# Kernel optimization log

Hardware: AMD Instinct MI355X
Metric: run time of the kernel (lower is better)

## Reference

```python
import jax, jax.numpy as jnp
import numpy as np

# dims per init_kwargs / input_specs
B, C, H, W = 8, 256, 56, 56
K = 3            # kernel_size
S = 1            # stride
D = 1            # dilation
HEAD = 1
MID = int(C * 0.2)   # se_ratio bottleneck = 51
GAIN = float(np.sqrt(2.0))  # calculate_gain('relu')


def setup_inputs() -> dict:
    key = jax.random.key(0)
    ks = jax.random.split(key, 6)
    sc = 0.05
    return {
        "x": jax.random.normal(ks[0], (B, C, H, W), jnp.float32),
        # channel branch: 1x1 convs stored as dense matrices
        "w1": jax.random.normal(ks[1], (MID, C), jnp.float32) * sc,
        "b1": jnp.zeros((MID,), jnp.float32),
        "w2": jax.random.normal(ks[2], (C * K * K, MID), jnp.float32) * sc,
        "b2": jnp.zeros((C * K * K,), jnp.float32),
        # spatial branch: 1x1 conv c -> head*k^2
        "ws": jax.random.normal(ks[3], (HEAD * K * K, C), jnp.float32) * sc,
        "bs": jnp.zeros((HEAD * K * K,), jnp.float32),
        # FilterNorm running_std parameter (channel branch): randn * gain/k
        "fn_std": jax.random.normal(ks[4], (C * K * K,), jnp.float32) * (GAIN / K),
    }


def _ddf_mul(x, cf, sf):
    """Decoupled dynamic filter, 'mul' combine.
    x: (B,C,H,W), cf: (B,C,K,K) channel filter, sf: (B,K*K,Ho,Wo) spatial filter.
    out[b,c,i,j] = sum_{u,v} x[b,c, i*S+(u-(K-1)/2)*D, j*S+(v-(K-1)/2)*D] * cf[b,c,u,v] * sf[b,u*K+v,i,j]
    Accumulate over the K*K taps to avoid materializing the unfolded tensor."""
    p = D * (K - 1) // 2
    xp = jnp.pad(x, ((0, 0), (0, 0), (p, p), (p, p)))
    Ho, Wo = H // S, W // S
    out = jnp.zeros((B, C, Ho, Wo), x.dtype)
    for u in range(K):
        for v in range(K):
            patch = xp[:, :, u * D:u * D + S * Ho:S, v * D:v * D + S * Wo:S]
            out = out + patch * cf[:, :, u, v][:, :, None, None] * sf[:, u * K + v][:, None]
    return out


def reference(x, w1, b1, w2, b2, ws, bs, fn_std):
    # ---- channel branch: SE-style filter generation ----
    pooled = x.mean((2, 3))                                  # (B,C) global avg pool
    y = jax.nn.relu(pooled @ w1.T + b1)                      # (B,MID)
    y = (y @ w2.T + b2).reshape(B, C, K * K)                 # (B,C,K^2)
    # FilterNorm 'channel': normalize over K^2 (torch std -> ddof=1), learned std
    y = (y - y.mean(-1, keepdims=True)) / (y.std(-1, ddof=1, keepdims=True) + 1e-10)
    cf = (y.reshape(B, C * K * K) * fn_std).reshape(B, C, K, K)
    # ---- spatial branch: 1x1 conv (stride S) + FilterNorm 'spatial' ----
    xs = x[:, :, ::S, ::S]
    sf = jnp.einsum('bchw,nc->bnhw', xs, ws) + bs[None, :, None, None]  # (B,K^2,Ho,Wo)
    sf = sf.reshape(B, HEAD, K * K, H // S, W // S)
    sf = (sf - sf.mean(2, keepdims=True)) / (sf.std(2, ddof=1, keepdims=True) + 1e-10)
    sf = sf.reshape(B, HEAD * K * K, H // S, W // S) * (GAIN / K)
    # ---- fused per-pixel gather-multiply-reduce (head=1 -> no group reshape) ----
    return _ddf_mul(x, cf, sf)
```

## Files before the change

kernel.cpp:

```cpp
#include <hip/hip_runtime.h>
#include <math.h>

#define BB   8
#define CC   256
#define HH   56
#define WW   56
#define KK   3
#define MIDN 51
#define NTAP (KK*KK)
#define CKK  (CC*NTAP)
#define HW   (HH*WW)
#define NCH  8
#define CPC  (CC/NCH)
#define PBLK 13

__global__ __launch_bounds__(256) void pool_kernel(const float* __restrict__ x,
                                                   float* __restrict__ pooled) {
    int bc = blockIdx.x;
    const float* xp = x + (size_t)bc * HW;
    int t = threadIdx.x;
    float s = 0.f;
    for (int idx = t; idx < HW; idx += 256) s += xp[idx];
    for (int off = 32; off > 0; off >>= 1) s += __shfl_down(s, off, 64);
    __shared__ float red[4];
    int wave = t >> 6, lane = t & 63;
    if (lane == 0) red[wave] = s;
    __syncthreads();
    if (t == 0) pooled[bc] = (red[0] + red[1] + red[2] + red[3]) * (1.0f / HW);
}

__global__ __launch_bounds__(320) void mlp_kernel(const float* __restrict__ pooled,
                                                  const float* __restrict__ w1,
                                                  const float* __restrict__ b1,
                                                  const float* __restrict__ w2,
                                                  const float* __restrict__ b2,
                                                  const float* __restrict__ fn_std,
                                                  float* __restrict__ cf) {
    int blk = blockIdx.x;
    int b = blk >> 3, chunk = blk & 7;
    int c0 = chunk * 32;
    int t = threadIdx.x;
    __shared__ float ps[CC];
    __shared__ float y1[MIDN];
    __shared__ float y2s[32 * NTAP];
    if (t < CC) ps[t] = pooled[b * CC + t];
    __syncthreads();
    if (t < MIDN) {
        float acc = b1[t];
        const float* wr = w1 + t * CC;
        for (int c2 = 0; c2 < CC; ++c2) acc += ps[c2] * wr[c2];
        y1[t] = fmaxf(acc, 0.f);
    }
    __syncthreads();
    if (t < 32 * NTAP) {
        int cl = t / NTAP, q = t - cl * NTAP;
        int row = (c0 + cl) * NTAP + q;
        float acc = b2[row];
        const float* r = w2 + (size_t)row * MIDN;
        for (int m = 0; m < MIDN; ++m) acc += y1[m] * r[m];
        y2s[t] = acc;
    }
    __syncthreads();
    if (t < 32) {
        int c = c0 + t;
        float y2[NTAP];
        #pragma unroll
        for (int q = 0; q < NTAP; ++q) y2[q] = y2s[t * NTAP + q];
        float mean = 0.f;
        #pragma unroll
        for (int q = 0; q < NTAP; ++q) mean += y2[q];
        mean *= (1.f / NTAP);
        float var = 0.f;
        #pragma unroll
        for (int q = 0; q < NTAP; ++q) { float d = y2[q] - mean; var += d * d; }
        float inv = 1.f / (sqrtf(var * (1.f / (NTAP - 1))) + 1e-10f);
        #pragma unroll
        for (int q = 0; q < NTAP; ++q) {
            int idx = c * NTAP + q;
            cf[(size_t)b * CKK + idx] = (y2[q] - mean) * inv * fn_std[idx];
        }
    }
}

__global__ __launch_bounds__(256) void sfA_kernel(const float* __restrict__ x,
                                                  const float* __restrict__ ws,
                                                  float* __restrict__ partial) {
    int blk = blockIdx.x;
    int pb = blk % PBLK;
    int tmp = blk / PBLK;
    int chunk = tmp % NCH;
    int b = tmp / NCH;
    int t = threadIdx.x;
    __shared__ float wss[NTAP][CPC];
    for (int idx = t; idx < NTAP * CPC; idx += 256) {
        int n = idx / CPC, c = idx - n * CPC;
        wss[n][c] = ws[n * CC + chunk * CPC + c];
    }
    __syncthreads();
    int p = pb * 256 + t;
    if (p >= HW) return;
    float acc[NTAP];
    #pragma unroll
    for (int n = 0; n < NTAP; ++n) acc[n] = 0.f;
    const float* xp = x + ((size_t)(b * CC + chunk * CPC)) * HW + p;
    for (int c = 0; c < CPC; ++c) {
        float xv = xp[(size_t)c * HW];
        #pragma unroll
        for (int n = 0; n < NTAP; ++n) acc[n] += xv * wss[n][c];
    }
    float* pp = partial + ((size_t)((b * NCH + chunk) * NTAP)) * HW + p;
    #pragma unroll
    for (int n = 0; n < NTAP; ++n) pp[(size_t)n * HW] = acc[n];
}

__global__ __launch_bounds__(256) void sfB_kernel(const float* __restrict__ partial,
                                                  const float* __restrict__ bs,
                                                  float* __restrict__ sf) {
    int blk = blockIdx.x;
    int b = blk / PBLK, pb = blk % PBLK;
    int p = pb * 256 + threadIdx.x;
    if (p >= HW) return;
    float acc[NTAP];
    #pragma unroll
    for (int n = 0; n < NTAP; ++n) acc[n] = bs[n];
    const float* pp = partial + ((size_t)(b * NCH)) * NTAP * HW + p;
    for (int chunk = 0; chunk < NCH; ++chunk)
        #pragma unroll
        for (int n = 0; n < NTAP; ++n)
            acc[n] += pp[((size_t)(chunk * NTAP + n)) * HW];
    float mean = 0.f;
    #pragma unroll
    for (int n = 0; n < NTAP; ++n) mean += acc[n];
    mean *= (1.f / NTAP);
    float var = 0.f;
    #pragma unroll
    for (int n = 0; n < NTAP; ++n) { float d = acc[n] - mean; var += d * d; }
    float inv = 0.47140452079103173f /
                (sqrtf(var * (1.f / (NTAP - 1))) + 1e-10f);
    #pragma unroll
    for (int n = 0; n < NTAP; ++n)
        sf[((size_t)(b * NTAP + n)) * HW + p] = (acc[n] - mean) * inv;
}

__global__ __launch_bounds__(256) void ddf_kernel(const float* __restrict__ x,
                                                  const float* __restrict__ cf,
                                                  const float* __restrict__ sf,
                                                  float* __restrict__ out) {
    int bc = blockIdx.x;
    int b = bc / CC, c = bc % CC;
    int t = threadIdx.x;
    __shared__ float xt[58 * 58];
    for (int idx = t; idx < 58 * 58; idx += 256) xt[idx] = 0.f;
    __syncthreads();
    const float* xp = x + (size_t)bc * HW;
    for (int idx = t; idx < HW; idx += 256) {
        int r = idx / WW, col = idx - r * WW;
        xt[(r + 1) * 58 + col + 1] = xp[idx];
    }
    float cf9[NTAP];
    const float* cfp = cf + (size_t)b * CKK + c * NTAP;
    #pragma unroll
    for (int n = 0; n < NTAP; ++n) cf9[n] = cfp[n];
    __syncthreads();
    const float* sfb = sf + (size_t)b * NTAP * HW;
    float* op = out + (size_t)bc * HW;
    for (int idx = t; idx < HW; idx += 256) {
        int i = idx / WW, j = idx - (idx / WW) * WW;
        float acc = 0.f;
        #pragma unroll
        for (int u = 0; u < KK; ++u)
            #pragma unroll
            for (int v = 0; v < KK; ++v) {
                int n = u * KK + v;
                acc += xt[(i + u) * 58 + (j + v)] * cf9[n] * sfb[(size_t)n * HW + idx];
            }
        op[idx] = acc;
    }
}

extern "C" void kernel_launch(void* const* d_in, const int* in_sizes, int n_in,
                              void* d_out, int out_size, void* d_ws, size_t ws_size,
                              hipStream_t stream) {
    const float* x      = (const float*)d_in[0];
    const float* w1     = (const float*)d_in[1];
    const float* b1     = (const float*)d_in[2];
    const float* w2     = (const float*)d_in[3];
    const float* b2     = (const float*)d_in[4];
    const float* ws     = (const float*)d_in[5];
    const float* bs     = (const float*)d_in[6];
    const float* fn_std = (const float*)d_in[7];
    float* out = (float*)d_out;

    float* wsf     = (float*)d_ws;
    float* pooled  = wsf;
    float* cf      = wsf + 2048;
    float* sf      = wsf + 2048 + 18432;
    float* partial = wsf + 2048 + 18432 + 225792;

    pool_kernel<<<BB * CC, 256, 0, stream>>>(x, pooled);
    sfA_kernel<<<BB * NCH * PBLK, 256, 0, stream>>>(x, ws, partial);
    mlp_kernel<<<BB * NCH, 320, 0, stream>>>(pooled, w1, b1, w2, b2, fn_std, cf);
    sfB_kernel<<<BB * PBLK, 256, 0, stream>>>(partial, bs, sf);
    ddf_kernel<<<BB * CC, 256, 0, stream>>>(x, cf, sf, out);
}
```

Before: 141.4 us.

## Fuse global pooling into spatial-filter pass and merge MLP with sfB kernel

The global average pool is now computed as per-block partial sums inside the spatial 1x1-conv pass, so x is read once for both instead of twice. The MLP and the spatial-filter normalisation run as independent block ranges of a single launch, which cuts the launch count from five to three. The MLP blocks also stage their w2 slice in shared memory with float4 loads. In exchange, every channel iteration now does a wave shuffle reduction, and the combined kernel uses a large shared allocation that can lower occupancy for the sfB blocks.

```diff
diff --git a/kernel.cpp b/kernel.cpp
--- a/kernel.cpp
+++ b/kernel.cpp
@@ -14,138 +14,159 @@
 #define CPC  (CC/NCH)
 #define PBLK 13
 
-__global__ __launch_bounds__(256) void pool_kernel(const float* __restrict__ x,
-                                                   float* __restrict__ pooled) {
-    int bc = blockIdx.x;
-    const float* xp = x + (size_t)bc * HW;
-    int t = threadIdx.x;
-    float s = 0.f;
-    for (int idx = t; idx < HW; idx += 256) s += xp[idx];
-    for (int off = 32; off > 0; off >>= 1) s += __shfl_down(s, off, 64);
-    __shared__ float red[4];
-    int wave = t >> 6, lane = t & 63;
-    if (lane == 0) red[wave] = s;
-    __syncthreads();
-    if (t == 0) pooled[bc] = (red[0] + red[1] + red[2] + red[3]) * (1.0f / HW);
-}
-
-__global__ __launch_bounds__(320) void mlp_kernel(const float* __restrict__ pooled,
-                                                  const float* __restrict__ w1,
-                                                  const float* __restrict__ b1,
-                                                  const float* __restrict__ w2,
-                                                  const float* __restrict__ b2,
-                                                  const float* __restrict__ fn_std,
-                                                  float* __restrict__ cf) {
-    int blk = blockIdx.x;
-    int b = blk >> 3, chunk = blk & 7;
-    int c0 = chunk * 32;
-    int t = threadIdx.x;
-    __shared__ float ps[CC];
-    __shared__ float y1[MIDN];
-    __shared__ float y2s[32 * NTAP];
-    if (t < CC) ps[t] = pooled[b * CC + t];
-    __syncthreads();
-    if (t < MIDN) {
-        float acc = b1[t];
-        const float* wr = w1 + t * CC;
-        for (int c2 = 0; c2 < CC; ++c2) acc += ps[c2] * wr[c2];
-        y1[t] = fmaxf(acc, 0.f);
-    }
-    __syncthreads();
-    if (t < 32 * NTAP) {
-        int cl = t / NTAP, q = t - cl * NTAP;
-        int row = (c0 + cl) * NTAP + q;
-        float acc = b2[row];
-        const float* r = w2 + (size_t)row * MIDN;
-        for (int m = 0; m < MIDN; ++m) acc += y1[m] * r[m];
-        y2s[t] = acc;
-    }
-    __syncthreads();
-    if (t < 32) {
-        int c = c0 + t;
-        float y2[NTAP];
-        #pragma unroll
-        for (int q = 0; q < NTAP; ++q) y2[q] = y2s[t * NTAP + q];
-        float mean = 0.f;
-        #pragma unroll
-        for (int q = 0; q < NTAP; ++q) mean += y2[q];
-        mean *= (1.f / NTAP);
-        float var = 0.f;
-        #pragma unroll
-        for (int q = 0; q < NTAP; ++q) { float d = y2[q] - mean; var += d * d; }
-        float inv = 1.f / (sqrtf(var * (1.f / (NTAP - 1))) + 1e-10f);
-        #pragma unroll
-        for (int q = 0; q < NTAP; ++q) {
-            int idx = c * NTAP + q;
-            cf[(size_t)b * CKK + idx] = (y2[q] - mean) * inv * fn_std[idx];
-        }
-    }
-}
-
-__global__ __launch_bounds__(256) void sfA_kernel(const float* __restrict__ x,
-                                                  const float* __restrict__ ws,
-                                                  float* __restrict__ partial) {
+__global__ __launch_bounds__(256) void k_sfpool(const float* __restrict__ x,
+                                                const float* __restrict__ ws,
+                                                float* __restrict__ partial,
+                                                float* __restrict__ poolpart) {
     int blk = blockIdx.x;
     int pb = blk % PBLK;
     int tmp = blk / PBLK;
     int chunk = tmp % NCH;
     int b = tmp / NCH;
     int t = threadIdx.x;
+    int wave = t >> 6, lane = t & 63;
     __shared__ float wss[NTAP][CPC];
+    __shared__ float wsum[4][CPC];
     for (int idx = t; idx < NTAP * CPC; idx += 256) {
         int n = idx / CPC, c = idx - n * CPC;
         wss[n][c] = ws[n * CC + chunk * CPC + c];
     }
     __syncthreads();
     int p = pb * 256 + t;
-    if (p >= HW) return;
+    bool act = (p < HW);
     float acc[NTAP];
     #pragma unroll
     for (int n = 0; n < NTAP; ++n) acc[n] = 0.f;
     const float* xp = x + ((size_t)(b * CC + chunk * CPC)) * HW + p;
     for (int c = 0; c < CPC; ++c) {
-        float xv = xp[(size_t)c * HW];
+        float xv = act ? xp[(size_t)c * HW] : 0.f;
         #pragma unroll
         for (int n = 0; n < NTAP; ++n) acc[n] += xv * wss[n][c];
-    }
-    float* pp = partial + ((size_t)((b * NCH + chunk) * NTAP)) * HW + p;
-    #pragma unroll
-    for (int n = 0; n < NTAP; ++n) pp[(size_t)n * HW] = acc[n];
-}
-
-__global__ __launch_bounds__(256) void sfB_kernel(const float* __restrict__ partial,
-                                                  const float* __restrict__ bs,
-                                                  float* __restrict__ sf) {
+        float s = xv;
+        s += __shfl_down(s, 32, 64);
+        s += __shfl_down(s, 16, 64);
+        s += __shfl_down(s, 8, 64);
+        s += __shfl_down(s, 4, 64);
+        s += __shfl_down(s, 2, 64);
+        s += __shfl_down(s, 1, 64);
+        if (lane == 0) wsum[wave][c] = s;
+    }
+    __syncthreads();
+    if (t < CPC) {
+        float psum = wsum[0][t] + wsum[1][t] + wsum[2][t] + wsum[3][t];
+        poolpart[((size_t)((b * NCH + chunk) * PBLK + pb)) * CPC + t] = psum;
+    }
+    if (act) {
+        float* pp = partial + ((size_t)((b * NCH + chunk) * NTAP)) * HW + p;
+        #pragma unroll
+        for (int n = 0; n < NTAP; ++n) pp[(size_t)n * HW] = acc[n];
+    }
+}
+
+#define MLPBLK (BB*NCH)
+#define W2CHUNK (CPC*NTAP*MIDN)
+__global__ __launch_bounds__(256) void k_mlp_sfB(const float* __restrict__ poolpart,
+                                                 const float* __restrict__ w1,
+                                                 const float* __restrict__ b1,
+                                                 const float* __restrict__ w2,
+                                                 const float* __restrict__ b2,
+                                                 const float* __restrict__ fn_std,
+                                                 const float* __restrict__ partial,
+                                                 const float* __restrict__ bs,
+                                                 float* __restrict__ cf,
+                                                 float* __restrict__ sf) {
+    __shared__ float smem[W2CHUNK + 256 + 64 + CPC * NTAP];
+    float* w2s = smem;
+    float* ps  = smem + W2CHUNK;
+    float* y1  = ps + 256;
+    float* y2s = y1 + 64;
     int blk = blockIdx.x;
-    int b = blk / PBLK, pb = blk % PBLK;
-    int p = pb * 256 + threadIdx.x;
-    if (p >= HW) return;
-    float acc[NTAP];
-    #pragma unroll
-    for (int n = 0; n < NTAP; ++n) acc[n] = bs[n];
-    const float* pp = partial + ((size_t)(b * NCH)) * NTAP * HW + p;
-    for (int chunk = 0; chunk < NCH; ++chunk)
+    int t = threadIdx.x;
+    if (blk < MLPBLK) {
+        int b = blk >> 3, chunk = blk & 7;
+        int c0 = chunk * CPC;
+        const float4* w2v = (const float4*)(w2 + (size_t)chunk * W2CHUNK);
+        float4* w2s4 = (float4*)w2s;
+        for (int i = t; i < W2CHUNK / 4; i += 256) w2s4[i] = w2v[i];
+        {
+            int chunkp = t >> 5, cl = t & 31;
+            float s = 0.f;
+            const float* pp = poolpart + ((size_t)(b * NCH + chunkp) * PBLK) * CPC + cl;
+            #pragma unroll
+            for (int pb = 0; pb < PBLK; ++pb) s += pp[pb * CPC];
+            ps[t] = s * (1.0f / HW);
+        }
+        __syncthreads();
+        if (t < MIDN) {
+            float acc = b1[t];
+            const float* wr = w1 + t * CC;
+            for (int c2 = 0; c2 < CC; ++c2) acc += ps[c2] * wr[c2];
+            y1[t] = fmaxf(acc, 0.f);
+        }
+        __syncthreads();
+        #pragma unroll
+        for (int base = 0; base < 512; base += 256) {
+            int idx = base + t;
+            if (idx < CPC * NTAP) {
+                float acc = b2[c0 * NTAP + idx];
+                const float* r = w2s + idx * MIDN;
+                #pragma unroll 3
+                for (int m = 0; m < MIDN; ++m) acc += y1[m] * r[m];
+                y2s[idx] = acc;
+            }
+        }
+        __syncthreads();
+        if (t < CPC) {
+            int c = c0 + t;
+            float y2[NTAP];
+            #pragma unroll
+            for (int q = 0; q < NTAP; ++q) y2[q] = y2s[t * NTAP + q];
+            float mean = 0.f;
+            #pragma unroll
+            for (int q = 0; q < NTAP; ++q) mean += y2[q];
+            mean *= (1.f / NTAP);
+            float var = 0.f;
+            #pragma unroll
+            for (int q = 0; q < NTAP; ++q) { float d = y2[q] - mean; var += d * d; }
+            float inv = 1.f / (sqrtf(var * (1.f / (NTAP - 1))) + 1e-10f);
+            #pragma unroll
+            for (int q = 0; q < NTAP; ++q) {
+                int idx = c * NTAP + q;
+                cf[(size_t)b * CKK + idx] = (y2[q] - mean) * inv * fn_std[idx];
+            }
+        }
+    } else {
+        int sblk = blk - MLPBLK;
+        int b = sblk / PBLK, pb = sblk % PBLK;
+        int p = pb * 256 + t;
+        if (p >= HW) return;
+        float acc[NTAP];
+        #pragma unroll
+        for (int n = 0; n < NTAP; ++n) acc[n] = bs[n];
+        const float* pp = partial + ((size_t)(b * NCH)) * NTAP * HW + p;
+        for (int chunk = 0; chunk < NCH; ++chunk)
+            #pragma unroll
+            for (int n = 0; n < NTAP; ++n)
+                acc[n] += pp[((size_t)(chunk * NTAP + n)) * HW];
+        float mean = 0.f;
+        #pragma unroll
+        for (int n = 0; n < NTAP; ++n) mean += acc[n];
+        mean *= (1.f / NTAP);
+        float var = 0.f;
+        #pragma unroll
+        for (int n = 0; n < NTAP; ++n) { float d = acc[n] - mean; var += d * d; }
+        float inv = 0.47140452079103173f /
+                    (sqrtf(var * (1.f / (NTAP - 1))) + 1e-10f);
         #pragma unroll
         for (int n = 0; n < NTAP; ++n)
-            acc[n] += pp[((size_t)(chunk * NTAP + n)) * HW];
-    float mean = 0.f;
-    #pragma unroll
-    for (int n = 0; n < NTAP; ++n) mean += acc[n];
-    mean *= (1.f / NTAP);
-    float var = 0.f;
-    #pragma unroll
-    for (int n = 0; n < NTAP; ++n) { float d = acc[n] - mean; var += d * d; }
-    float inv = 0.47140452079103173f /
-                (sqrtf(var * (1.f / (NTAP - 1))) + 1e-10f);
-    #pragma unroll
-    for (int n = 0; n < NTAP; ++n)
-        sf[((size_t)(b * NTAP + n)) * HW + p] = (acc[n] - mean) * inv;
-}
-
-__global__ __launch_bounds__(256) void ddf_kernel(const float* __restrict__ x,
-                                                  const float* __restrict__ cf,
-                                                  const float* __restrict__ sf,
-                                                  float* __restrict__ out) {
+            sf[((size_t)(b * NTAP + n)) * HW + p] = (acc[n] - mean) * inv;
+    }
+}
+
+__global__ __launch_bounds__(256) void k_ddf(const float* __restrict__ x,
+                                             const float* __restrict__ cf,
+                                             const float* __restrict__ sf,
+                                             float* __restrict__ out) {
     int bc = blockIdx.x;
     int b = bc / CC, c = bc % CC;
     int t = threadIdx.x;
@@ -191,15 +212,14 @@
     const float* fn_std = (const float*)d_in[7];
     float* out = (float*)d_out;
 
-    float* wsf     = (float*)d_ws;
-    float* pooled  = wsf;
-    float* cf      = wsf + 2048;
-    float* sf      = wsf + 2048 + 18432;
-    float* partial = wsf + 2048 + 18432 + 225792;
-
-    pool_kernel<<<BB * CC, 256, 0, stream>>>(x, pooled);
-    sfA_kernel<<<BB * NCH * PBLK, 256, 0, stream>>>(x, ws, partial);
-    mlp_kernel<<<BB * NCH, 320, 0, stream>>>(pooled, w1, b1, w2, b2, fn_std, cf);
-    sfB_kernel<<<BB * PBLK, 256, 0, stream>>>(partial, bs, sf);
-    ddf_kernel<<<BB * CC, 256, 0, stream>>>(x, cf, sf, out);
-}
+    float* wsf      = (float*)d_ws;
+    float* cf       = wsf;
+    float* sf       = cf + 18432;
+    float* poolpart = sf + 225792;
+    float* partial  = poolpart + 26624;
+
+    k_sfpool<<<BB * NCH * PBLK, 256, 0, stream>>>(x, ws, partial, poolpart);
+    k_mlp_sfB<<<MLPBLK + BB * PBLK, 256, 0, stream>>>(poolpart, w1, b1, w2, b2,
+                                                      fn_std, partial, bs, cf, sf);
+    k_ddf<<<BB * CC, 256, 0, stream>>>(x, cf, sf, out);
+}
```

Result: faster. 134.1 us (-5.2%).
